# Kernel optimization log

Measured on AMD Instinct MI355X. Metric: run time of the kernel, lower is better.

The kernel has to match this reference:

```python
import jax, jax.numpy as jnp
import numpy as np

KDIM = 8192
EPS = 1e-8  # F.cosine_similarity default eps


def _encoder(x, W1, b1, W2, b2, W3, b3):
    # x: [..., KDIM] -> [..., 128]; Linear(KDIM,512)->ReLU->Linear(512,256)->ReLU->Linear(256,128)
    h = jax.nn.relu(x @ W1 + b1)
    h = jax.nn.relu(h @ W2 + b2)
    return h @ W3 + b3


def setup_inputs() -> dict:
    key = jax.random.key(0)
    ks = jax.random.split(key, 16)

    def lin(k, fan_in, fan_out):
        bound = 1.0 / np.sqrt(fan_in)
        kw, kb = jax.random.split(k)
        W = jax.random.uniform(kw, (fan_in, fan_out), jnp.float32, -bound, bound)
        b = jax.random.uniform(kb, (fan_out,), jnp.float32, -bound, bound)
        return W, b

    W1, b1 = lin(ks[0], KDIM, 512)
    W2, b2 = lin(ks[1], 512, 256)
    W3, b3 = lin(ks[2], 256, 128)
    Wi1, bi1 = lin(ks[3], 128 + 6, 64)
    Wi2, bi2 = lin(ks[4], 64, 32)
    Wi3, bi3 = lin(ks[5], 32, 1)

    return {
        "new_knowledge": jax.random.normal(ks[6], (KDIM,), jnp.float32),
        "existing_knowledge": jax.random.normal(ks[7], (10, KDIM), jnp.float32),
        "math_metrics": jax.random.uniform(ks[8], (6,), jnp.float32),
        "W1": W1, "b1": b1, "W2": W2, "b2": b2, "W3": W3, "b3": b3,
        "Wi1": Wi1, "bi1": bi1, "Wi2": Wi2, "bi2": bi2, "Wi3": Wi3, "bi3": bi3,
    }


def reference(new_knowledge, existing_knowledge, math_metrics,
              W1, b1, W2, b2, W3, b3, Wi1, bi1, Wi2, bi2, Wi3, bi3):
    # Encode new knowledge: [128]
    new_enc = _encoder(new_knowledge, W1, b1, W2, b2, W3, b3)
    # Batched encode of the (up to 10) existing knowledge vectors: [10, 128]
    ex_enc = _encoder(existing_knowledge, W1, b1, W2, b2, W3, b3)

    # Per-item geometric distance (L2 norm of difference)
    diff = new_enc[None, :] - ex_enc                     # [10, 128]
    geo_dist = jnp.sqrt(jnp.sum(diff * diff, axis=-1))   # [10]

    # Per-item cosine similarity with torch eps clamping
    new_n = jnp.maximum(jnp.linalg.norm(new_enc), EPS)
    ex_n = jnp.maximum(jnp.linalg.norm(ex_enc, axis=-1), EPS)  # [10]
    cos = (ex_enc @ new_enc) / (new_n * ex_n)            # [10]

    avg_consistency = jnp.mean(geo_dist - cos)

    # Mathematical-constraint integrator MLP on [128 + 6]
    combined = jnp.concatenate([new_enc, math_metrics])  # [134]
    h = jax.nn.relu(combined @ Wi1 + bi1)
    h = jax.nn.relu(h @ Wi2 + bi2)
    quality = h @ Wi3 + bi3                              # [1]

    integration_loss = jnp.exp(-quality)                 # [1]
    total = jnp.squeeze(avg_consistency + integration_loss)
    return total
```

## Files before the change

kernel.cpp:

```cpp
#include <hip/hip_runtime.h>
#include <math.h>

#define EPS 1e-8f

__device__ __forceinline__ float wredsum(float v) {
#pragma unroll
  for (int o = 32; o > 0; o >>= 1) v += __shfl_down(v, o, 64);
  return v;
}

__device__ __forceinline__ void fma8(const float4* w, const float4 a,
                                     const float4 b, float4& c) {
  const float xs[8] = {a.x, a.y, a.z, a.w, b.x, b.y, b.z, b.w};
#pragma unroll
  for (int i = 0; i < 8; ++i) {
    c.x = fmaf(xs[i], w[i].x, c.x);
    c.y = fmaf(xs[i], w[i].y, c.y);
    c.z = fmaf(xs[i], w[i].z, c.z);
    c.w = fmaf(xs[i], w[i].w, c.w);
  }
}

__global__ __launch_bounds__(256, 2) void k_l1(const float* __restrict__ xn,
                                               const float* __restrict__ xe,
                                               const float* __restrict__ W1,
                                               float* __restrict__ p1,
                                               int* __restrict__ bars) {
  if (blockIdx.x == 0 && blockIdx.y == 0 && threadIdx.x == 0) bars[0] = 0;
  __shared__ float red[11 * 32 * 36];
  const int cg  = threadIdx.x & 7;
  const int ks  = threadIdx.x >> 3;
  const int col = blockIdx.x * 32 + cg * 4;
  const int k0  = blockIdx.y * 256 + ks * 8;

  float4 w[8];
#pragma unroll
  for (int i = 0; i < 8; ++i)
    w[i] = *(const float4*)&W1[(size_t)(k0 + i) * 512 + col];

  float4 acc[11];
#pragma unroll
  for (int r = 0; r < 11; ++r) acc[r] = make_float4(0.f, 0.f, 0.f, 0.f);

  {
    const float4 a = *(const float4*)&xn[k0];
    const float4 b = *(const float4*)&xn[k0 + 4];
    fma8(w, a, b, acc[0]);
  }
#pragma unroll
  for (int r = 0; r < 10; ++r) {
    const float4 a = *(const float4*)&xe[r * 8192 + k0];
    const float4 b = *(const float4*)&xe[r * 8192 + k0 + 4];
    fma8(w, a, b, acc[r + 1]);
  }

#pragma unroll
  for (int r = 0; r < 11; ++r)
    *(float4*)&red[(r * 32 + ks) * 36 + cg * 4] = acc[r];
  __syncthreads();

  for (int o = threadIdx.x; o < 352; o += 256) {
    const int r = o >> 5, c = o & 31;
    float s = 0.f;
#pragma unroll
    for (int k = 0; k < 32; ++k) s += red[(r * 32 + k) * 36 + c];
    p1[((size_t)blockIdx.y * 11 + r) * 512 + blockIdx.x * 32 + c] = s;
  }
}

__global__ __launch_bounds__(1024) void k_tail(
    const float* __restrict__ p1, const float* __restrict__ b1,
    const float* __restrict__ W2, const float* __restrict__ b2,
    const float* __restrict__ W3, const float* __restrict__ b3,
    const float* __restrict__ mm,
    const float* __restrict__ Wi1, const float* __restrict__ bi1,
    const float* __restrict__ Wi2, const float* __restrict__ bi2,
    const float* __restrict__ Wi3, const float* __restrict__ bi3,
    float* __restrict__ p2, int* __restrict__ bars, float* __restrict__ out) {
  __shared__ float h1sl[11 * 64];
  __shared__ float red[11264];
  __shared__ float h2s[11 * 256];
  __shared__ __align__(16) float wi1s[134 * 64];
  __shared__ float encs[1408];
  __shared__ float comb[134];
  __shared__ float h1b[64];
  __shared__ int won;
  const int t = threadIdx.x;
  const int j = blockIdx.x;

  if (t < 704) {
    const int r = t >> 6, kk = t & 63;
    const int col = j * 64 + kk;
    float s = b1[col];
#pragma unroll
    for (int ch = 0; ch < 32; ++ch) s += p1[(size_t)ch * 5632 + r * 512 + col];
    h1sl[r * 64 + kk] = fmaxf(s, 0.f);
  }
  __syncthreads();

  {
    const int col = t & 255, g = t >> 8;
    float acc[11];
#pragma unroll
    for (int r = 0; r < 11; ++r) acc[r] = 0.f;
#pragma unroll
    for (int kk = 0; kk < 16; ++kk) {
      const int kl = g * 16 + kk;
      const float w = W2[(size_t)(j * 64 + kl) * 256 + col];
#pragma unroll
      for (int r = 0; r < 11; ++r) acc[r] = fmaf(h1sl[r * 64 + kl], w, acc[r]);
    }
#pragma unroll
    for (int r = 0; r < 11; ++r) red[(g * 11 + r) * 256 + col] = acc[r];
  }
  __syncthreads();
  for (int o = t; o < 2816; o += 1024) {
    const int col = o & 255, r = o >> 8;
    p2[j * 2816 + o] = red[r * 256 + col] + red[(11 + r) * 256 + col] +
                       red[(22 + r) * 256 + col] + red[(33 + r) * 256 + col];
  }

  __syncthreads();
  if (t == 0) {
    __threadfence();
    const int old = __hip_atomic_fetch_add(bars, 1, __ATOMIC_ACQ_REL,
                                           __HIP_MEMORY_SCOPE_AGENT);
    won = (old == 7);
    if (won) __threadfence();
  }
  __syncthreads();
  if (!won) return;

  for (int i = t; i < 2144; i += 1024)
    *(float4*)&wi1s[i * 4] = *(const float4*)&Wi1[(size_t)i * 4];
  for (int o = t; o < 2816; o += 1024) {
    float s = b2[o & 255];
#pragma unroll
    for (int jj = 0; jj < 8; ++jj) s += p2[jj * 2816 + o];
    h2s[o] = fmaxf(s, 0.f);
  }
  __syncthreads();

  {
    const int c = t & 127, g = t >> 7;
    float acc[11];
#pragma unroll
    for (int r = 0; r < 11; ++r) acc[r] = 0.f;
#pragma unroll
    for (int kk = 0; kk < 32; ++kk) {
      const int k = g * 32 + kk;
      const float w = W3[(size_t)k * 128 + c];
#pragma unroll
      for (int r = 0; r < 11; ++r) acc[r] = fmaf(h2s[r * 256 + k], w, acc[r]);
    }
#pragma unroll
    for (int r = 0; r < 11; ++r) red[(g * 11 + r) * 128 + c] = acc[r];
  }
  __syncthreads();
  for (int o = t; o < 1408; o += 1024) {
    const int c = o & 127, r = o >> 7;
    float s = b3[c];
#pragma unroll
    for (int g = 0; g < 8; ++g) s += red[(g * 11 + r) * 128 + c];
    encs[o] = s;
  }
  __syncthreads();

  float consist = 0.f;
  float n0 = 0.f, n1 = 0.f;
  if (t < 64) {
    n0 = encs[t]; n1 = encs[64 + t];
    comb[t] = n0; comb[64 + t] = n1;
    if (t < 6) comb[128 + t] = mm[t];
  }
  __syncthreads();
  if (t < 64) {
    const float nn = wredsum(n0 * n0 + n1 * n1);
#pragma unroll
    for (int r = 1; r <= 10; ++r) {
      const float e0 = encs[r * 128 + t];
      const float e1 = encs[r * 128 + 64 + t];
      const float d0 = e0 - n0, d1 = e1 - n1;
      const float g  = wredsum(d0 * d0 + d1 * d1);
      const float q  = wredsum(e0 * e0 + e1 * e1);
      const float dd = wredsum(e0 * n0 + e1 * n1);
      if (t == 0) {
        const float geo = sqrtf(g);
        const float den = fmaxf(sqrtf(nn), EPS) * fmaxf(sqrtf(q), EPS);
        consist += geo - dd / den;
      }
    }
  } else if (t < 128) {
    const int tt = t - 64;
    float h = bi1[tt];
#pragma unroll 4
    for (int k = 0; k < 134; ++k) h = fmaf(comb[k], wi1s[k * 64 + tt], h);
    h1b[tt] = fmaxf(h, 0.f);
  }
  __syncthreads();
  if (t < 64) {
    float part = 0.f;
    if (t < 32) {
      float h2 = bi2[t];
#pragma unroll 8
      for (int k = 0; k < 64; ++k) h2 = fmaf(h1b[k], Wi2[k * 32 + t], h2);
      part = fmaxf(h2, 0.f) * Wi3[t];
    }
    const float qual = wredsum(part);
    if (t == 0) out[0] = consist * 0.1f + expf(-(qual + bi3[0]));
  }
}

extern "C" void kernel_launch(void* const* d_in, const int* in_sizes, int n_in,
                              void* d_out, int out_size, void* d_ws, size_t ws_size,
                              hipStream_t stream) {
  (void)in_sizes; (void)n_in; (void)out_size; (void)ws_size;
  const float* xn  = (const float*)d_in[0];
  const float* xe  = (const float*)d_in[1];
  const float* mm  = (const float*)d_in[2];
  const float* W1  = (const float*)d_in[3];
  const float* b1  = (const float*)d_in[4];
  const float* W2  = (const float*)d_in[5];
  const float* b2  = (const float*)d_in[6];
  const float* W3  = (const float*)d_in[7];
  const float* b3  = (const float*)d_in[8];
  const float* Wi1 = (const float*)d_in[9];
  const float* bi1 = (const float*)d_in[10];
  const float* Wi2 = (const float*)d_in[11];
  const float* bi2 = (const float*)d_in[12];
  const float* Wi3 = (const float*)d_in[13];
  const float* bi3 = (const float*)d_in[14];
  float* out = (float*)d_out;

  char* ws = (char*)d_ws;
  float* p1   = (float*)(ws);
  float* p2   = (float*)(ws + 720896);
  int*   bars = (int*)  (ws + 811008);

  hipLaunchKernelGGL(k_l1,   dim3(16, 32), dim3(256),  0, stream, xn, xe, W1, p1, bars);
  hipLaunchKernelGGL(k_tail, dim3(8),      dim3(1024), 0, stream,
                     p1, b1, W2, b2, W3, b3, mm,
                     Wi1, bi1, Wi2, bi2, Wi3, bi3, p2, bars, out);
}
```

Baseline: 114.8 us.

## Collapse tail into single block, drop atomic last-block barrier and p2 round-trip

Replaces the 8-block tail kernel, which used a global atomic counter to elect a last block, with one 1024-thread block that does the whole layer-1 reduction plus the layer-2 and layer-3 matvecs. Split-K partial sums are now combined with wavefront shuffles, and activations are stored in an interleaved shared-memory layout, so the shared reduction buffers and the global p2 workspace are no longer needed. The aim is to remove the cross-block atomic and fence handshake and the extra global traffic. The cost is that one block now streams all of W2 (512 KB) and reduces all of p1 by itself, which may lengthen the serial tail.

```diff
diff --git a/kernel.cpp b/kernel.cpp
--- a/kernel.cpp
+++ b/kernel.cpp
@@ -24,9 +24,7 @@
 __global__ __launch_bounds__(256, 2) void k_l1(const float* __restrict__ xn,
                                                const float* __restrict__ xe,
                                                const float* __restrict__ W1,
-                                               float* __restrict__ p1,
-                                               int* __restrict__ bars) {
-  if (blockIdx.x == 0 && blockIdx.y == 0 && threadIdx.x == 0) bars[0] = 0;
+                                               float* __restrict__ p1) {
   __shared__ float red[11 * 32 * 36];
   const int cg  = threadIdx.x & 7;
   const int ks  = threadIdx.x >> 3;
@@ -68,7 +66,7 @@
   }
 }
 
-__global__ __launch_bounds__(1024) void k_tail(
+__global__ __launch_bounds__(1024) void k_tail1(
     const float* __restrict__ p1, const float* __restrict__ b1,
     const float* __restrict__ W2, const float* __restrict__ b2,
     const float* __restrict__ W3, const float* __restrict__ b3,
@@ -76,93 +74,70 @@
     const float* __restrict__ Wi1, const float* __restrict__ bi1,
     const float* __restrict__ Wi2, const float* __restrict__ bi2,
     const float* __restrict__ Wi3, const float* __restrict__ bi3,
-    float* __restrict__ p2, int* __restrict__ bars, float* __restrict__ out) {
-  __shared__ float h1sl[11 * 64];
-  __shared__ float red[11264];
-  __shared__ float h2s[11 * 256];
-  __shared__ __align__(16) float wi1s[134 * 64];
+    float* __restrict__ out) {
+  __shared__ float h1[5632];
+  __shared__ float h2[2816];
   __shared__ float encs[1408];
   __shared__ float comb[134];
   __shared__ float h1b[64];
-  __shared__ int won;
   const int t = threadIdx.x;
-  const int j = blockIdx.x;
-
-  if (t < 704) {
-    const int r = t >> 6, kk = t & 63;
-    const int col = j * 64 + kk;
+
+  for (int o = t; o < 5632; o += 1024) {
+    const int col = o & 511;
     float s = b1[col];
-#pragma unroll
-    for (int ch = 0; ch < 32; ++ch) s += p1[(size_t)ch * 5632 + r * 512 + col];
-    h1sl[r * 64 + kk] = fmaxf(s, 0.f);
+#pragma unroll 8
+    for (int ch = 0; ch < 32; ++ch) s += p1[(size_t)ch * 5632 + o];
+    h1[(o & ~511) | ((col & 127) << 2) | (col >> 7)] = fmaxf(s, 0.f);
   }
   __syncthreads();
 
   {
-    const int col = t & 255, g = t >> 8;
+    const int col = t >> 2, kg = t & 3;
     float acc[11];
 #pragma unroll
     for (int r = 0; r < 11; ++r) acc[r] = 0.f;
-#pragma unroll
-    for (int kk = 0; kk < 16; ++kk) {
-      const int kl = g * 16 + kk;
-      const float w = W2[(size_t)(j * 64 + kl) * 256 + col];
-#pragma unroll
-      for (int r = 0; r < 11; ++r) acc[r] = fmaf(h1sl[r * 64 + kl], w, acc[r]);
-    }
-#pragma unroll
-    for (int r = 0; r < 11; ++r) red[(g * 11 + r) * 256 + col] = acc[r];
-  }
-  __syncthreads();
-  for (int o = t; o < 2816; o += 1024) {
-    const int col = o & 255, r = o >> 8;
-    p2[j * 2816 + o] = red[r * 256 + col] + red[(11 + r) * 256 + col] +
-                       red[(22 + r) * 256 + col] + red[(33 + r) * 256 + col];
-  }
-
-  __syncthreads();
-  if (t == 0) {
-    __threadfence();
-    const int old = __hip_atomic_fetch_add(bars, 1, __ATOMIC_ACQ_REL,
-                                           __HIP_MEMORY_SCOPE_AGENT);
-    won = (old == 7);
-    if (won) __threadfence();
-  }
-  __syncthreads();
-  if (!won) return;
-
-  for (int i = t; i < 2144; i += 1024)
-    *(float4*)&wi1s[i * 4] = *(const float4*)&Wi1[(size_t)i * 4];
-  for (int o = t; o < 2816; o += 1024) {
-    float s = b2[o & 255];
-#pragma unroll
-    for (int jj = 0; jj < 8; ++jj) s += p2[jj * 2816 + o];
-    h2s[o] = fmaxf(s, 0.f);
+#pragma unroll 8
+    for (int kk = 0; kk < 128; ++kk) {
+      const int k = kg * 128 + kk;
+      const float w = W2[(size_t)k * 256 + col];
+      const int hk = (kk << 2) | kg;
+#pragma unroll
+      for (int r = 0; r < 11; ++r) acc[r] = fmaf(h1[r * 512 + hk], w, acc[r]);
+    }
+    const float bb = b2[col];
+#pragma unroll
+    for (int r = 0; r < 11; ++r) {
+      float v = acc[r];
+      v += __shfl_down(v, 1, 64);
+      v += __shfl_down(v, 2, 64);
+      if (kg == 0)
+        h2[r * 256 + ((col & 31) << 3) + (col >> 5)] = fmaxf(v + bb, 0.f);
+    }
   }
   __syncthreads();
 
   {
-    const int c = t & 127, g = t >> 7;
+    const int c = t >> 3, kg = t & 7;
     float acc[11];
 #pragma unroll
     for (int r = 0; r < 11; ++r) acc[r] = 0.f;
-#pragma unroll
+#pragma unroll 4
     for (int kk = 0; kk < 32; ++kk) {
-      const int k = g * 32 + kk;
+      const int k = kg * 32 + kk;
       const float w = W3[(size_t)k * 128 + c];
-#pragma unroll
-      for (int r = 0; r < 11; ++r) acc[r] = fmaf(h2s[r * 256 + k], w, acc[r]);
-    }
-#pragma unroll
-    for (int r = 0; r < 11; ++r) red[(g * 11 + r) * 128 + c] = acc[r];
-  }
-  __syncthreads();
-  for (int o = t; o < 1408; o += 1024) {
-    const int c = o & 127, r = o >> 7;
-    float s = b3[c];
-#pragma unroll
-    for (int g = 0; g < 8; ++g) s += red[(g * 11 + r) * 128 + c];
-    encs[o] = s;
+      const int hk = (kk << 3) | kg;
+#pragma unroll
+      for (int r = 0; r < 11; ++r) acc[r] = fmaf(h2[r * 256 + hk], w, acc[r]);
+    }
+    const float bb = b3[c];
+#pragma unroll
+    for (int r = 0; r < 11; ++r) {
+      float v = acc[r];
+      v += __shfl_down(v, 1, 64);
+      v += __shfl_down(v, 2, 64);
+      v += __shfl_down(v, 4, 64);
+      if (kg == 0) encs[r * 128 + c] = v + bb;
+    }
   }
   __syncthreads();
 
@@ -194,17 +169,17 @@
     const int tt = t - 64;
     float h = bi1[tt];
 #pragma unroll 4
-    for (int k = 0; k < 134; ++k) h = fmaf(comb[k], wi1s[k * 64 + tt], h);
+    for (int k = 0; k < 134; ++k) h = fmaf(comb[k], Wi1[(size_t)k * 64 + tt], h);
     h1b[tt] = fmaxf(h, 0.f);
   }
   __syncthreads();
   if (t < 64) {
     float part = 0.f;
     if (t < 32) {
-      float h2 = bi2[t];
+      float hh = bi2[t];
 #pragma unroll 8
-      for (int k = 0; k < 64; ++k) h2 = fmaf(h1b[k], Wi2[k * 32 + t], h2);
-      part = fmaxf(h2, 0.f) * Wi3[t];
+      for (int k = 0; k < 64; ++k) hh = fmaf(h1b[k], Wi2[k * 32 + t], hh);
+      part = fmaxf(hh, 0.f) * Wi3[t];
     }
     const float qual = wredsum(part);
     if (t == 0) out[0] = consist * 0.1f + expf(-(qual + bi3[0]));
@@ -232,13 +207,10 @@
   const float* bi3 = (const float*)d_in[14];
   float* out = (float*)d_out;
 
-  char* ws = (char*)d_ws;
-  float* p1   = (float*)(ws);
-  float* p2   = (float*)(ws + 720896);
-  int*   bars = (int*)  (ws + 811008);
-
-  hipLaunchKernelGGL(k_l1,   dim3(16, 32), dim3(256),  0, stream, xn, xe, W1, p1, bars);
-  hipLaunchKernelGGL(k_tail, dim3(8),      dim3(1024), 0, stream,
+  float* p1 = (float*)d_ws;
+
+  hipLaunchKernelGGL(k_l1,    dim3(16, 32), dim3(256),  0, stream, xn, xe, W1, p1);
+  hipLaunchKernelGGL(k_tail1, dim3(1),      dim3(1024), 0, stream,
                      p1, b1, W2, b2, W3, b3, mm,
-                     Wi1, bi1, Wi2, bi2, Wi3, bi3, p2, bars, out);
-}
+                     Wi1, bi1, Wi2, bi2, Wi3, bi3, out);
+}
```

After: 156.5 us. 36.3% more time.

## Spread tail layers across 64 blocks with two-stage atomic barriers and prefetch

Applied to the files above, without the earlier changes.

The tail kernel goes from 8 blocks of 1024 threads to 64 blocks of 256. Layer 2 is split by k-group and column-group, and the last 16 arriving blocks spin-wait and each compute 8 columns of layer 3. A second atomic counter picks one final block to run the consistency and integrator MLP. The change also prefetches W3/Wi1/Wi2 into cache through dead loads and marks W1/W2 reads as nontemporal. This aims to raise parallelism in the serial tail, at the cost of a spin-wait that assumes all 64 blocks are co-resident, plus an extra global round trip for the encodings.

```diff
diff --git a/kernel.cpp b/kernel.cpp
--- a/kernel.cpp
+++ b/kernel.cpp
@@ -2,6 +2,7 @@
 #include <math.h>
 
 #define EPS 1e-8f
+typedef float f32x4 __attribute__((ext_vector_type(4)));
 
 __device__ __forceinline__ float wredsum(float v) {
 #pragma unroll
@@ -9,15 +10,15 @@
   return v;
 }
 
-__device__ __forceinline__ void fma8(const float4* w, const float4 a,
-                                     const float4 b, float4& c) {
-  const float xs[8] = {a.x, a.y, a.z, a.w, b.x, b.y, b.z, b.w};
+__device__ __forceinline__ void fma8v(const f32x4* w, const f32x4 a,
+                                      const f32x4 b, f32x4& c) {
+  const float xs[8] = {a[0], a[1], a[2], a[3], b[0], b[1], b[2], b[3]};
 #pragma unroll
   for (int i = 0; i < 8; ++i) {
-    c.x = fmaf(xs[i], w[i].x, c.x);
-    c.y = fmaf(xs[i], w[i].y, c.y);
-    c.z = fmaf(xs[i], w[i].z, c.z);
-    c.w = fmaf(xs[i], w[i].w, c.w);
+    c[0] = fmaf(xs[i], w[i][0], c[0]);
+    c[1] = fmaf(xs[i], w[i][1], c[1]);
+    c[2] = fmaf(xs[i], w[i][2], c[2]);
+    c[3] = fmaf(xs[i], w[i][3], c[3]);
   }
 }
 
@@ -26,37 +27,40 @@
                                                const float* __restrict__ W1,
                                                float* __restrict__ p1,
                                                int* __restrict__ bars) {
-  if (blockIdx.x == 0 && blockIdx.y == 0 && threadIdx.x == 0) bars[0] = 0;
+  if (blockIdx.x == 0 && blockIdx.y == 0 && threadIdx.x == 0) {
+    bars[0] = 0; bars[1] = 0;
+  }
   __shared__ float red[11 * 32 * 36];
   const int cg  = threadIdx.x & 7;
   const int ks  = threadIdx.x >> 3;
   const int col = blockIdx.x * 32 + cg * 4;
   const int k0  = blockIdx.y * 256 + ks * 8;
 
-  float4 w[8];
+  f32x4 w[8];
 #pragma unroll
   for (int i = 0; i < 8; ++i)
-    w[i] = *(const float4*)&W1[(size_t)(k0 + i) * 512 + col];
-
-  float4 acc[11];
-#pragma unroll
-  for (int r = 0; r < 11; ++r) acc[r] = make_float4(0.f, 0.f, 0.f, 0.f);
-
-  {
-    const float4 a = *(const float4*)&xn[k0];
-    const float4 b = *(const float4*)&xn[k0 + 4];
-    fma8(w, a, b, acc[0]);
+    w[i] = __builtin_nontemporal_load(
+        (const f32x4*)&W1[(size_t)(k0 + i) * 512 + col]);
+
+  f32x4 acc[11];
+#pragma unroll
+  for (int r = 0; r < 11; ++r) acc[r] = (f32x4){0.f, 0.f, 0.f, 0.f};
+
+  {
+    const f32x4 a = *(const f32x4*)&xn[k0];
+    const f32x4 b = *(const f32x4*)&xn[k0 + 4];
+    fma8v(w, a, b, acc[0]);
   }
 #pragma unroll
   for (int r = 0; r < 10; ++r) {
-    const float4 a = *(const float4*)&xe[r * 8192 + k0];
-    const float4 b = *(const float4*)&xe[r * 8192 + k0 + 4];
-    fma8(w, a, b, acc[r + 1]);
+    const f32x4 a = *(const f32x4*)&xe[r * 8192 + k0];
+    const f32x4 b = *(const f32x4*)&xe[r * 8192 + k0 + 4];
+    fma8v(w, a, b, acc[r + 1]);
   }
 
 #pragma unroll
   for (int r = 0; r < 11; ++r)
-    *(float4*)&red[(r * 32 + ks) * 36 + cg * 4] = acc[r];
+    *(f32x4*)&red[(r * 32 + ks) * 36 + cg * 4] = acc[r];
   __syncthreads();
 
   for (int o = threadIdx.x; o < 352; o += 256) {
@@ -68,7 +72,7 @@
   }
 }
 
-__global__ __launch_bounds__(1024) void k_tail(
+__global__ __launch_bounds__(256) void k_tail(
     const float* __restrict__ p1, const float* __restrict__ b1,
     const float* __restrict__ W2, const float* __restrict__ b2,
     const float* __restrict__ W3, const float* __restrict__ b3,
@@ -76,94 +80,126 @@
     const float* __restrict__ Wi1, const float* __restrict__ bi1,
     const float* __restrict__ Wi2, const float* __restrict__ bi2,
     const float* __restrict__ Wi3, const float* __restrict__ bi3,
-    float* __restrict__ p2, int* __restrict__ bars, float* __restrict__ out) {
-  __shared__ float h1sl[11 * 64];
-  __shared__ float red[11264];
+    float* __restrict__ p2, float* __restrict__ enc,
+    int* __restrict__ bars, float* __restrict__ out) {
+  __shared__ float h1s[11 * 64];
+  __shared__ float redA[8 * 11 * 33];
   __shared__ float h2s[11 * 256];
-  __shared__ __align__(16) float wi1s[134 * 64];
+  __shared__ float redB[32 * 11 * 9];
   __shared__ float encs[1408];
   __shared__ float comb[134];
   __shared__ float h1b[64];
-  __shared__ int won;
+  __shared__ int tick;
   const int t = threadIdx.x;
-  const int j = blockIdx.x;
-
-  if (t < 704) {
-    const int r = t >> 6, kk = t & 63;
-    const int col = j * 64 + kk;
+  const int b = blockIdx.x;
+  const int kg = b >> 3, cg = b & 7;
+
+  float dead = 0.f;
+  {
+    const int g = b * 256 + t;
+    if (g < 8192) { f32x4 x = ((const f32x4*)W3)[g];  dead += x[0]; }
+    if (g < 2144) { f32x4 x = ((const f32x4*)Wi1)[g]; dead += x[1]; }
+    if (g < 512)  { f32x4 x = ((const f32x4*)Wi2)[g]; dead += x[2]; }
+  }
+
+  for (int o = t; o < 704; o += 256) {
+    const int r = o >> 6, k = o & 63;
+    const int col = kg * 64 + k;
     float s = b1[col];
 #pragma unroll
-    for (int ch = 0; ch < 32; ++ch) s += p1[(size_t)ch * 5632 + r * 512 + col];
-    h1sl[r * 64 + kk] = fmaxf(s, 0.f);
-  }
-  __syncthreads();
-
-  {
-    const int col = t & 255, g = t >> 8;
+    for (int ch = 0; ch < 32; ++ch) s += p1[(size_t)(ch * 11 + r) * 512 + col];
+    h1s[r * 64 + k] = fmaxf(s, 0.f);
+  }
+  __syncthreads();
+
+  {
+    const int c = t & 31, ks = t >> 5;
+    const int col = cg * 32 + c;
     float acc[11];
 #pragma unroll
     for (int r = 0; r < 11; ++r) acc[r] = 0.f;
 #pragma unroll
-    for (int kk = 0; kk < 16; ++kk) {
-      const int kl = g * 16 + kk;
-      const float w = W2[(size_t)(j * 64 + kl) * 256 + col];
-#pragma unroll
-      for (int r = 0; r < 11; ++r) acc[r] = fmaf(h1sl[r * 64 + kl], w, acc[r]);
-    }
-#pragma unroll
-    for (int r = 0; r < 11; ++r) red[(g * 11 + r) * 256 + col] = acc[r];
-  }
-  __syncthreads();
-  for (int o = t; o < 2816; o += 1024) {
-    const int col = o & 255, r = o >> 8;
-    p2[j * 2816 + o] = red[r * 256 + col] + red[(11 + r) * 256 + col] +
-                       red[(22 + r) * 256 + col] + red[(33 + r) * 256 + col];
+    for (int kk = 0; kk < 8; ++kk) {
+      const int kl = ks * 8 + kk;
+      const float w =
+          __builtin_nontemporal_load(&W2[(size_t)(kg * 64 + kl) * 256 + col]);
+#pragma unroll
+      for (int r = 0; r < 11; ++r) acc[r] = fmaf(h1s[r * 64 + kl], w, acc[r]);
+    }
+#pragma unroll
+    for (int r = 0; r < 11; ++r) redA[(ks * 11 + r) * 33 + c] = acc[r];
+  }
+  asm volatile("" ::"v"(dead));
+  __syncthreads();
+  for (int o = t; o < 352; o += 256) {
+    const int r = o >> 5, c = o & 31;
+    float s = 0.f;
+#pragma unroll
+    for (int k = 0; k < 8; ++k) s += redA[(k * 11 + r) * 33 + c];
+    p2[(size_t)(kg * 11 + r) * 256 + cg * 32 + c] = s;
   }
 
   __syncthreads();
   if (t == 0) {
     __threadfence();
-    const int old = __hip_atomic_fetch_add(bars, 1, __ATOMIC_ACQ_REL,
-                                           __HIP_MEMORY_SCOPE_AGENT);
-    won = (old == 7);
-    if (won) __threadfence();
-  }
-  __syncthreads();
-  if (!won) return;
-
-  for (int i = t; i < 2144; i += 1024)
-    *(float4*)&wi1s[i * 4] = *(const float4*)&Wi1[(size_t)i * 4];
-  for (int o = t; o < 2816; o += 1024) {
-    float s = b2[o & 255];
-#pragma unroll
-    for (int jj = 0; jj < 8; ++jj) s += p2[jj * 2816 + o];
-    h2s[o] = fmaxf(s, 0.f);
-  }
-  __syncthreads();
-
-  {
-    const int c = t & 127, g = t >> 7;
+    tick = __hip_atomic_fetch_add(&bars[0], 1, __ATOMIC_ACQ_REL,
+                                  __HIP_MEMORY_SCOPE_AGENT);
+  }
+  __syncthreads();
+  const int rank = tick - 48;
+  if (rank < 0) return;
+  if (t == 0) {
+    while (__hip_atomic_load(&bars[0], __ATOMIC_RELAXED,
+                             __HIP_MEMORY_SCOPE_AGENT) < 64)
+      __builtin_amdgcn_s_sleep(1);
+    __threadfence();
+  }
+  __syncthreads();
+
+  for (int o = t; o < 2816; o += 256) {
+    const int k = o & 255, r = o >> 8;
+    float s = b2[k];
+#pragma unroll
+    for (int g = 0; g < 8; ++g) s += p2[(size_t)(g * 11 + r) * 256 + k];
+    h2s[r * 256 + k] = fmaxf(s, 0.f);
+  }
+  __syncthreads();
+  {
+    const int j = t & 7, ks = t >> 3;
     float acc[11];
 #pragma unroll
     for (int r = 0; r < 11; ++r) acc[r] = 0.f;
 #pragma unroll
-    for (int kk = 0; kk < 32; ++kk) {
-      const int k = g * 32 + kk;
-      const float w = W3[(size_t)k * 128 + c];
+    for (int kk = 0; kk < 8; ++kk) {
+      const int k = ks * 8 + kk;
+      const float w = W3[(size_t)k * 128 + rank * 8 + j];
 #pragma unroll
       for (int r = 0; r < 11; ++r) acc[r] = fmaf(h2s[r * 256 + k], w, acc[r]);
     }
 #pragma unroll
-    for (int r = 0; r < 11; ++r) red[(g * 11 + r) * 128 + c] = acc[r];
-  }
-  __syncthreads();
-  for (int o = t; o < 1408; o += 1024) {
-    const int c = o & 127, r = o >> 7;
-    float s = b3[c];
-#pragma unroll
-    for (int g = 0; g < 8; ++g) s += red[(g * 11 + r) * 128 + c];
-    encs[o] = s;
-  }
+    for (int r = 0; r < 11; ++r) redB[(ks * 11 + r) * 9 + j] = acc[r];
+  }
+  __syncthreads();
+  if (t < 88) {
+    const int r = t >> 3, j = t & 7;
+    float s = b3[rank * 8 + j];
+#pragma unroll
+    for (int k = 0; k < 32; ++k) s += redB[(k * 11 + r) * 9 + j];
+    enc[r * 128 + rank * 8 + j] = s;
+  }
+
+  __syncthreads();
+  if (t == 0) {
+    __threadfence();
+    tick = __hip_atomic_fetch_add(&bars[1], 1, __ATOMIC_ACQ_REL,
+                                  __HIP_MEMORY_SCOPE_AGENT);
+  }
+  __syncthreads();
+  if (tick != 15) return;
+  if (t == 0) __threadfence();
+  __syncthreads();
+
+  for (int i = t; i < 352; i += 256) ((f32x4*)encs)[i] = ((const f32x4*)enc)[i];
   __syncthreads();
 
   float consist = 0.f;
@@ -194,17 +230,17 @@
     const int tt = t - 64;
     float h = bi1[tt];
 #pragma unroll 4
-    for (int k = 0; k < 134; ++k) h = fmaf(comb[k], wi1s[k * 64 + tt], h);
+    for (int k = 0; k < 134; ++k) h = fmaf(comb[k], Wi1[(size_t)k * 64 + tt], h);
     h1b[tt] = fmaxf(h, 0.f);
   }
   __syncthreads();
   if (t < 64) {
     float part = 0.f;
     if (t < 32) {
-      float h2 = bi2[t];
+      float hh = bi2[t];
 #pragma unroll 8
-      for (int k = 0; k < 64; ++k) h2 = fmaf(h1b[k], Wi2[k * 32 + t], h2);
-      part = fmaxf(h2, 0.f) * Wi3[t];
+      for (int k = 0; k < 64; ++k) hh = fmaf(h1b[k], Wi2[k * 32 + t], hh);
+      part = fmaxf(hh, 0.f) * Wi3[t];
     }
     const float qual = wredsum(part);
     if (t == 0) out[0] = consist * 0.1f + expf(-(qual + bi3[0]));
@@ -235,10 +271,11 @@
   char* ws = (char*)d_ws;
   float* p1   = (float*)(ws);
   float* p2   = (float*)(ws + 720896);
-  int*   bars = (int*)  (ws + 811008);
-
-  hipLaunchKernelGGL(k_l1,   dim3(16, 32), dim3(256),  0, stream, xn, xe, W1, p1, bars);
-  hipLaunchKernelGGL(k_tail, dim3(8),      dim3(1024), 0, stream,
+  float* enc  = (float*)(ws + 811008);
+  int*   bars = (int*)  (ws + 816640);
+
+  hipLaunchKernelGGL(k_l1,   dim3(16, 32), dim3(256), 0, stream, xn, xe, W1, p1, bars);
+  hipLaunchKernelGGL(k_tail, dim3(64),     dim3(256), 0, stream,
                      p1, b1, W2, b2, W3, b3, mm,
-                     Wi1, bi1, Wi2, bi2, Wi3, bi3, p2, bars, out);
-}
+                     Wi1, bi1, Wi2, bi2, Wi3, bi3, p2, enc, bars, out);
+}
```

New measurement: 129.4 us. 12.7% more time.

## Split tail kernel across 16 blocks with staged layer-3 across 4 blocks

Applied to the files above, without the earlier changes.

The tail kernel now runs layer 2 across 16 blocks instead of 8, each handling 32 hidden rows. The last 4 blocks to arrive then spin-wait until all 16 have written their partials and split layer 3 by K, writing partial encodings to a new workspace buffer. A final block reduces those partials and runs the small MLP, reading Wi2 from LDS. W2 and W3 weights are loaded into registers before waiting on data, to hide latency. The cost is an extra global barrier stage with spin-waiting, which depends on all 16 blocks being resident at once.

```diff
diff --git a/kernel.cpp b/kernel.cpp
--- a/kernel.cpp
+++ b/kernel.cpp
@@ -2,6 +2,7 @@
 #include <math.h>
 
 #define EPS 1e-8f
+typedef float f32x4 __attribute__((ext_vector_type(4)));
 
 __device__ __forceinline__ float wredsum(float v) {
 #pragma unroll
@@ -26,7 +27,9 @@
                                                const float* __restrict__ W1,
                                                float* __restrict__ p1,
                                                int* __restrict__ bars) {
-  if (blockIdx.x == 0 && blockIdx.y == 0 && threadIdx.x == 0) bars[0] = 0;
+  if (blockIdx.x == 0 && blockIdx.y == 0 && threadIdx.x == 0) {
+    bars[0] = 0; bars[1] = 0;
+  }
   __shared__ float red[11 * 32 * 36];
   const int cg  = threadIdx.x & 7;
   const int ks  = threadIdx.x >> 3;
@@ -76,92 +79,135 @@
     const float* __restrict__ Wi1, const float* __restrict__ bi1,
     const float* __restrict__ Wi2, const float* __restrict__ bi2,
     const float* __restrict__ Wi3, const float* __restrict__ bi3,
-    float* __restrict__ p2, int* __restrict__ bars, float* __restrict__ out) {
-  __shared__ float h1sl[11 * 64];
-  __shared__ float red[11264];
-  __shared__ float h2s[11 * 256];
-  __shared__ __align__(16) float wi1s[134 * 64];
-  __shared__ float encs[1408];
-  __shared__ float comb[134];
-  __shared__ float h1b[64];
-  __shared__ int won;
+    float* __restrict__ p2, float* __restrict__ encp,
+    int* __restrict__ bars, float* __restrict__ out) {
+  __shared__ __align__(16) float smem[12368];
+  __shared__ int tick;
   const int t = threadIdx.x;
   const int j = blockIdx.x;
 
+  const int c = t & 255, kg = t >> 8;
+  float w2r[8];
+#pragma unroll
+  for (int kk = 0; kk < 8; ++kk)
+    w2r[kk] = W2[(size_t)(j * 32 + kg * 8 + kk) * 256 + c];
+
+  float* h1s = smem;
+  if (t < 352) {
+    const int r = t >> 5, cc = t & 31;
+    const int col = j * 32 + cc;
+    float s = b1[col];
+#pragma unroll
+    for (int ch = 0; ch < 32; ++ch) s += p1[(size_t)(ch * 11 + r) * 512 + col];
+    h1s[r * 32 + cc] = fmaxf(s, 0.f);
+  }
+  __syncthreads();
+
+  float* redA = smem + 1024;
+  {
+    float acc[11];
+#pragma unroll
+    for (int r = 0; r < 11; ++r) acc[r] = 0.f;
+#pragma unroll
+    for (int kk = 0; kk < 8; ++kk) {
+      const int kl = kg * 8 + kk;
+#pragma unroll
+      for (int r = 0; r < 11; ++r)
+        acc[r] = fmaf(h1s[r * 32 + kl], w2r[kk], acc[r]);
+    }
+#pragma unroll
+    for (int r = 0; r < 11; ++r) redA[(kg * 11 + r) * 256 + c] = acc[r];
+  }
+  __syncthreads();
+  for (int o = t; o < 2816; o += 1024) {
+    const int r = o >> 8, cc = o & 255;
+    p2[(size_t)j * 2816 + o] = redA[r * 256 + cc] + redA[(11 + r) * 256 + cc] +
+                               redA[(22 + r) * 256 + cc] +
+                               redA[(33 + r) * 256 + cc];
+  }
+
+  __syncthreads();
+  if (t == 0) {
+    __threadfence();
+    tick = __hip_atomic_fetch_add(&bars[0], 1, __ATOMIC_ACQ_REL,
+                                  __HIP_MEMORY_SCOPE_AGENT);
+  }
+  __syncthreads();
+  const int rank = tick;
+  if (rank < 12) return;
+  const int q = rank - 12;
+
+  const int c3 = t & 127, kg3 = t >> 7;
+  float w3r[8];
+#pragma unroll
+  for (int kk = 0; kk < 8; ++kk)
+    w3r[kk] = W3[(size_t)(q * 64 + kg3 * 8 + kk) * 128 + c3];
+
+  if (t == 0) {
+    while (__hip_atomic_load(&bars[0], __ATOMIC_RELAXED,
+                             __HIP_MEMORY_SCOPE_AGENT) < 16)
+      __builtin_amdgcn_s_sleep(1);
+    __threadfence();
+  }
+  __syncthreads();
+
+  float* h2q = smem;
   if (t < 704) {
     const int r = t >> 6, kk = t & 63;
-    const int col = j * 64 + kk;
-    float s = b1[col];
-#pragma unroll
-    for (int ch = 0; ch < 32; ++ch) s += p1[(size_t)ch * 5632 + r * 512 + col];
-    h1sl[r * 64 + kk] = fmaxf(s, 0.f);
-  }
-  __syncthreads();
-
+    const int col = q * 64 + kk;
+    float s = b2[col];
+#pragma unroll
+    for (int jj = 0; jj < 16; ++jj) s += p2[(size_t)jj * 2816 + r * 256 + col];
+    h2q[r * 64 + kk] = fmaxf(s, 0.f);
+  }
+  __syncthreads();
+  float* redB = smem + 1024;
   {
-    const int col = t & 255, g = t >> 8;
     float acc[11];
 #pragma unroll
     for (int r = 0; r < 11; ++r) acc[r] = 0.f;
 #pragma unroll
-    for (int kk = 0; kk < 16; ++kk) {
-      const int kl = g * 16 + kk;
-      const float w = W2[(size_t)(j * 64 + kl) * 256 + col];
-#pragma unroll
-      for (int r = 0; r < 11; ++r) acc[r] = fmaf(h1sl[r * 64 + kl], w, acc[r]);
-    }
-#pragma unroll
-    for (int r = 0; r < 11; ++r) red[(g * 11 + r) * 256 + col] = acc[r];
-  }
-  __syncthreads();
-  for (int o = t; o < 2816; o += 1024) {
-    const int col = o & 255, r = o >> 8;
-    p2[j * 2816 + o] = red[r * 256 + col] + red[(11 + r) * 256 + col] +
-                       red[(22 + r) * 256 + col] + red[(33 + r) * 256 + col];
+    for (int kk = 0; kk < 8; ++kk) {
+      const int kl = kg3 * 8 + kk;
+#pragma unroll
+      for (int r = 0; r < 11; ++r)
+        acc[r] = fmaf(h2q[r * 64 + kl], w3r[kk], acc[r]);
+    }
+#pragma unroll
+    for (int r = 0; r < 11; ++r) redB[(kg3 * 11 + r) * 128 + c3] = acc[r];
+  }
+  __syncthreads();
+  for (int o = t; o < 1408; o += 1024) {
+    const int r = o >> 7, cc = o & 127;
+    float s = 0.f;
+#pragma unroll
+    for (int g = 0; g < 8; ++g) s += redB[(g * 11 + r) * 128 + cc];
+    encp[(size_t)q * 1408 + o] = s;
   }
 
   __syncthreads();
   if (t == 0) {
     __threadfence();
-    const int old = __hip_atomic_fetch_add(bars, 1, __ATOMIC_ACQ_REL,
-                                           __HIP_MEMORY_SCOPE_AGENT);
-    won = (old == 7);
-    if (won) __threadfence();
-  }
-  __syncthreads();
-  if (!won) return;
-
+    tick = __hip_atomic_fetch_add(&bars[1], 1, __ATOMIC_ACQ_REL,
+                                  __HIP_MEMORY_SCOPE_AGENT);
+  }
+  __syncthreads();
+  if (tick != 3) return;
+  if (t == 0) __threadfence();
+  __syncthreads();
+
+  float* encs = smem;
+  float* wi1s = smem + 1536;
+  float* wi2s = smem + 10112;
+  float* comb = smem + 12160;
+  float* h1b  = smem + 12296;
   for (int i = t; i < 2144; i += 1024)
-    *(float4*)&wi1s[i * 4] = *(const float4*)&Wi1[(size_t)i * 4];
-  for (int o = t; o < 2816; o += 1024) {
-    float s = b2[o & 255];
-#pragma unroll
-    for (int jj = 0; jj < 8; ++jj) s += p2[jj * 2816 + o];
-    h2s[o] = fmaxf(s, 0.f);
-  }
-  __syncthreads();
-
-  {
-    const int c = t & 127, g = t >> 7;
-    float acc[11];
-#pragma unroll
-    for (int r = 0; r < 11; ++r) acc[r] = 0.f;
-#pragma unroll
-    for (int kk = 0; kk < 32; ++kk) {
-      const int k = g * 32 + kk;
-      const float w = W3[(size_t)k * 128 + c];
-#pragma unroll
-      for (int r = 0; r < 11; ++r) acc[r] = fmaf(h2s[r * 256 + k], w, acc[r]);
-    }
-#pragma unroll
-    for (int r = 0; r < 11; ++r) red[(g * 11 + r) * 128 + c] = acc[r];
-  }
-  __syncthreads();
+    ((f32x4*)wi1s)[i] = ((const f32x4*)Wi1)[i];
+  if (t < 512) ((f32x4*)wi2s)[t] = ((const f32x4*)Wi2)[t];
   for (int o = t; o < 1408; o += 1024) {
-    const int c = o & 127, r = o >> 7;
-    float s = b3[c];
-#pragma unroll
-    for (int g = 0; g < 8; ++g) s += red[(g * 11 + r) * 128 + c];
+    float s = b3[o & 127];
+#pragma unroll
+    for (int g = 0; g < 4; ++g) s += encp[(size_t)g * 1408 + o];
     encs[o] = s;
   }
   __syncthreads();
@@ -182,11 +228,11 @@
       const float e1 = encs[r * 128 + 64 + t];
       const float d0 = e0 - n0, d1 = e1 - n1;
       const float g  = wredsum(d0 * d0 + d1 * d1);
-      const float q  = wredsum(e0 * e0 + e1 * e1);
+      const float qq = wredsum(e0 * e0 + e1 * e1);
       const float dd = wredsum(e0 * n0 + e1 * n1);
       if (t == 0) {
         const float geo = sqrtf(g);
-        const float den = fmaxf(sqrtf(nn), EPS) * fmaxf(sqrtf(q), EPS);
+        const float den = fmaxf(sqrtf(nn), EPS) * fmaxf(sqrtf(qq), EPS);
         consist += geo - dd / den;
       }
     }
@@ -201,10 +247,10 @@
   if (t < 64) {
     float part = 0.f;
     if (t < 32) {
-      float h2 = bi2[t];
+      float hh = bi2[t];
 #pragma unroll 8
-      for (int k = 0; k < 64; ++k) h2 = fmaf(h1b[k], Wi2[k * 32 + t], h2);
-      part = fmaxf(h2, 0.f) * Wi3[t];
+      for (int k = 0; k < 64; ++k) hh = fmaf(h1b[k], wi2s[k * 32 + t], hh);
+      part = fmaxf(hh, 0.f) * Wi3[t];
     }
     const float qual = wredsum(part);
     if (t == 0) out[0] = consist * 0.1f + expf(-(qual + bi3[0]));
@@ -235,10 +281,11 @@
   char* ws = (char*)d_ws;
   float* p1   = (float*)(ws);
   float* p2   = (float*)(ws + 720896);
-  int*   bars = (int*)  (ws + 811008);
+  float* encp = (float*)(ws + 901120);
+  int*   bars = (int*)  (ws + 923648);
 
   hipLaunchKernelGGL(k_l1,   dim3(16, 32), dim3(256),  0, stream, xn, xe, W1, p1, bars);
-  hipLaunchKernelGGL(k_tail, dim3(8),      dim3(1024), 0, stream,
+  hipLaunchKernelGGL(k_tail, dim3(16),     dim3(1024), 0, stream,
                      p1, b1, W2, b2, W3, b3, mm,
-                     Wi1, bi1, Wi2, bi2, Wi3, bi3, p2, bars, out);
-}
+                     Wi1, bi1, Wi2, bi2, Wi3, bi3, p2, encp, bars, out);
+}
```

New measurement: 109.4 us (median of 2 runs). 1.05x faster.
